# Kernel optimization log

Measured on AMD Instinct MI355X. Metric: run time of the kernel, lower is better.

## Reference

```python
import jax, jax.numpy as jnp
import numpy as np

N_POINTS = 32
N_HEADS = 4
EMBED = 256
TAU = 2.0


def _grid_sample_bilinear(val, gx, gy):
    # val: [N, C, H, W]; gx, gy: [N, Q, P] normalized coords in [-1, 1]
    # bilinear, padding_mode='zeros', align_corners=False
    N, C, H, W = val.shape
    ix = (gx + 1.0) * (W * 0.5) - 0.5
    iy = (gy + 1.0) * (H * 0.5) - 0.5
    x0 = jnp.floor(ix)
    y0 = jnp.floor(iy)
    x1 = x0 + 1.0
    y1 = y0 + 1.0
    wx1 = ix - x0
    wx0 = 1.0 - wx1
    wy1 = iy - y0
    wy0 = 1.0 - wy1
    gather = jax.vmap(lambda v, yy, xx: v[:, yy, xx])  # per-image advanced-index gather
    out = jnp.zeros((N, C) + gx.shape[1:], dtype=val.dtype)
    for xs, ys, wx, wy in ((x0, y0, wx0, wy0), (x1, y0, wx1, wy0),
                           (x0, y1, wx0, wy1), (x1, y1, wx1, wy1)):
        m = ((xs >= 0) & (xs < W) & (ys >= 0) & (ys < H)).astype(val.dtype) * wx * wy
        xi = jnp.clip(xs, 0, W - 1).astype(jnp.int32)
        yi = jnp.clip(ys, 0, H - 1).astype(jnp.int32)
        out = out + gather(val, yi, xi) * m[:, None]
    return out  # [N, C, Q, P]


def setup_inputs() -> dict:
    key = jax.random.key(0)
    ks = jax.random.split(key, 18)
    B, L = 2, 1000
    lvl_hw = [(256, 256), (128, 128), (64, 64), (32, 32)]
    inp = {}
    for i, (h, w) in enumerate(lvl_hw):
        inp[f'value{i}'] = jax.random.normal(ks[i], (B, EMBED, h, w), jnp.float32)
    inp['query_content'] = jax.random.normal(ks[4], (B, L, EMBED), jnp.float32)
    img = 1024.0
    xy = jax.random.uniform(ks[5], (B, L, 2), minval=0.0, maxval=img)
    z = jax.random.uniform(ks[6], (B, L, 1), minval=4.0, maxval=6.5)
    r = jax.random.uniform(ks[7], (B, L, 1), minval=-0.8, maxval=0.8)
    th = jax.random.uniform(ks[8], (B, L, 1), minval=-np.pi, maxval=np.pi)
    inp['query_xyzrt'] = jnp.concatenate([xy, z, r, th], axis=-1).astype(jnp.float32)
    inp['strides'] = jnp.array([4, 8, 16, 32], jnp.int32)
    s = 0.02
    inp['W_off'] = jax.random.normal(ks[9], (EMBED, N_HEADS * N_POINTS * 3)) * s
    inp['b_off'] = jax.random.normal(ks[10], (N_HEADS * N_POINTS * 3,)) * 0.2
    inp['W_ca1'] = jax.random.normal(ks[11], (EMBED, EMBED // 4)) * s
    inp['W_ca2'] = jax.random.normal(ks[12], (EMBED // 4, EMBED)) * s
    inp['W_sa1'] = jax.random.normal(ks[13], (EMBED, EMBED // 4)) * s
    inp['W_sa2'] = jax.random.normal(ks[14], (EMBED // 4, N_HEADS * N_POINTS)) * s
    inp['W_out'] = jax.random.normal(ks[15], (EMBED * N_POINTS, EMBED)) * s
    inp['b_out'] = jnp.zeros((EMBED,), jnp.float32)
    return inp


def reference(value0, value1, value2, value3, query_content, query_xyzrt, strides,
              W_off, b_off, W_ca1, W_ca2, W_sa1, W_sa2, W_out, b_out):
    values = [value0, value1, value2, value3]
    B, L, _ = query_content.shape
    P = N_HEADS * N_POINTS
    G = N_HEADS
    ch = EMBED // G

    # ---- make_sample_points ----
    offset = (query_content @ W_off + b_off).reshape(B, L, P, 3)
    roi_cc = query_xyzrt[..., :2]                      # [B,L,2]
    scale = 2.0 ** query_xyzrt[..., 2:3]
    ratio = 2.0 ** jnp.concatenate([query_xyzrt[..., 3:4] * -0.5,
                                    query_xyzrt[..., 3:4] * 0.5], axis=-1)
    roi_wh = scale * ratio                             # [B,L,2]
    theta = query_xyzrt[..., 4]
    c, s = jnp.cos(theta), jnp.sin(theta)
    R = jnp.stack([jnp.stack([c, -s], -1), jnp.stack([s, c], -1)], -2)  # [B,L,2,2]
    off_xy = offset[..., :2] * roi_wh[:, :, None, :]
    rot_xy = jnp.einsum('blpj,blij->blpi', off_xy, R)  # offset @ R^T
    sample_xy = roi_cc[:, :, None, :] + rot_xy         # [B,L,P,2] absolute coords
    sample_z = query_xyzrt[..., 2][:, :, None] + offset[..., 2]  # [B,L,P]

    # ---- level weights: sigmoid(-(z - log2(stride))^2 / tau) ----
    grid = jnp.log2(strides.astype(sample_z.dtype))    # [n_levels]
    lvl_w = jax.nn.sigmoid(-((sample_z[..., None] - grid) ** 2) / TAU)  # [B,L,P,n_lvl]

    # ---- multi-level rotated deformable sampling ----
    sampling_value = jnp.zeros((B, L, G, N_POINTS, ch), query_content.dtype)
    for lvl, v in enumerate(values):
        H, W = v.shape[2], v.shape[3]
        stride_f = strides[lvl].astype(sample_xy.dtype)
        mapping = jnp.stack([W * stride_f, H * stride_f])  # (x_extent, y_extent)
        norm_xy = sample_xy / mapping * 2.0 - 1.0          # [B,L,P,2] in [-1,1]
        # split points into head groups: [B,L,G,pts,2] -> [B*G, L, pts, 2]
        g_xy = norm_xy.reshape(B, L, G, N_POINTS, 2).transpose(0, 2, 1, 3, 4).reshape(B * G, L, N_POINTS, 2)
        v_g = v.reshape(B * G, ch, H, W)
        out = _grid_sample_bilinear(v_g, g_xy[..., 0], g_xy[..., 1])  # [B*G, ch, L, pts]
        w = lvl_w[..., lvl].reshape(B, L, G, N_POINTS).transpose(0, 2, 1, 3).reshape(B * G, 1, L, N_POINTS)
        out = out * w
        sampling_value = sampling_value + out.reshape(B, G, ch, L, N_POINTS).transpose(0, 3, 1, 4, 2)

    # ---- channel / spatial attention gates ----
    ca = jax.nn.sigmoid(jax.nn.relu(query_content @ W_ca1) @ W_ca2)
    ca = ca.reshape(B, L, G, 1, ch)
    sa = jax.nn.sigmoid(jax.nn.relu(query_content @ W_sa1) @ W_sa2)
    sa = sa.reshape(B, L, G, N_POINTS, 1)
    out = sampling_value * ca * sa
    out = out.reshape(B, L, G * N_POINTS * ch) @ W_out + b_out
    return out + query_content
```

## Files before the change

### kernel.cpp

```cpp
#include <hip/hip_runtime.h>

#define NQ    2000
#define KDIM  8192
#define EMB   256
#define MPAD  2048
#define SPLITK 8

typedef __attribute__((ext_vector_type(8))) short bf16x8;
typedef __attribute__((ext_vector_type(4))) float f32x4;

__device__ __forceinline__ float sigf(float x) { return 1.0f / (1.0f + __expf(-x)); }

__device__ __forceinline__ unsigned short f2bf(float x) {
    union { float f; unsigned int u; } v; v.f = x;
    unsigned int r = v.u + 0x7fffu + ((v.u >> 16) & 1u);
    return (unsigned short)(r >> 16);
}
__device__ __forceinline__ float bf2f(unsigned short h) {
    union { unsigned int u; float f; } v; v.u = ((unsigned int)h) << 16; return v.f;
}

__global__ __launch_bounds__(256) void trans_kernel(
    const float* __restrict__ v0, const float* __restrict__ v1,
    const float* __restrict__ v2, const float* __restrict__ v3,
    unsigned short* __restrict__ vt0, unsigned short* __restrict__ vt1,
    unsigned short* __restrict__ vt2, unsigned short* __restrict__ vt3,
    const float* __restrict__ Wout, unsigned short* __restrict__ Wtb,
    const float* __restrict__ Woff, const float* __restrict__ Wca1,
    const float* __restrict__ Wsa1,
    unsigned short* __restrict__ WH, unsigned short* __restrict__ WL,
    const float* __restrict__ qc,
    unsigned short* __restrict__ qcH, unsigned short* __restrict__ qcL)
{
    __shared__ float tile[64][33];
    int bid = blockIdx.x;
    const int t = threadIdx.x;

    if (bid < 21760) {
        const float* v; unsigned short* vt; int H;
        if (bid < 16384)      { v = v0; vt = vt0; H = 256; }
        else if (bid < 20480) { bid -= 16384; v = v1; vt = vt1; H = 128; }
        else if (bid < 21504) { bid -= 20480; v = v2; vt = vt2; H = 64; }
        else                  { bid -= 21504; v = v3; vt = vt3; H = 32; }
        const int y  = bid % H;            bid /= H;
        const int xt = bid % (H >> 5);     bid /= (H >> 5);
        const int ct = bid & 3;
        const int b  = bid >> 2;
        const float* src = v + ((size_t)(b * 256 + ct * 64) * H + y) * H + xt * 32;
        const int xi = t & 31;
        #pragma unroll
        for (int i = 0; i < 8; i++) {
            const int c = (t >> 5) + i * 8;
            tile[c][xi] = src[(size_t)c * H * H + xi];
        }
        __syncthreads();
        unsigned short* dst = vt + (((size_t)(b * H + y) * H + xt * 32) * 256) + ct * 64;
        const int ci = (t & 31) * 2;
        #pragma unroll
        for (int i = 0; i < 4; i++) {
            const int x2 = (t >> 5) + i * 8;
            ushort2 pk;
            pk.x = f2bf(tile[ci][x2]);
            pk.y = f2bf(tile[ci + 1][x2]);
            *(ushort2*)(dst + (size_t)x2 * 256 + ci) = pk;
        }
    } else if (bid < 23808) {
        const int local = bid - 21760;
        const int k0 = (local & 255) * 32, n0 = (local >> 8) * 32;
        float (*tl)[33] = tile;
        #pragma unroll
        for (int i = 0; i < 4; i++) {
            const int ki = (t >> 5) + i * 8;
            tl[ki][t & 31] = Wout[(size_t)(k0 + ki) * 256 + n0 + (t & 31)];
        }
        __syncthreads();
        #pragma unroll
        for (int i = 0; i < 4; i++) {
            const int ni = (t >> 5) + i * 8;
            const int ki = t & 31;
            Wtb[(size_t)(n0 + ni) * KDIM + k0 + ki] = f2bf(tl[ki][ni]);
        }
    } else if (bid < 24320) {
        const int n = bid - 23808;
        float val;
        if (n < 384)      val = Woff[(size_t)t * 384 + n];
        else if (n < 448) val = Wca1[(size_t)t * 64 + (n - 384)];
        else              val = Wsa1[(size_t)t * 64 + (n - 448)];
        const unsigned short hh = f2bf(val);
        WH[(size_t)n * 256 + t] = hh;
        WL[(size_t)n * 256 + t] = f2bf(val - bf2f(hh));
    } else {
        const int q = bid - 24320;
        const float val = (q < NQ) ? qc[(size_t)q * 256 + t] : 0.f;
        const unsigned short hh = f2bf(val);
        qcH[(size_t)q * 256 + t] = hh;
        qcL[(size_t)q * 256 + t] = f2bf(val - bf2f(hh));
    }
}

__global__ __launch_bounds__(256) void gemmA_kernel(
    const unsigned short* __restrict__ qcH, const unsigned short* __restrict__ qcL,
    const unsigned short* __restrict__ WH,  const unsigned short* __restrict__ WL,
    float* __restrict__ Hout)
{
    const int m0 = blockIdx.x * 64;
    const int n0 = blockIdx.y * 64;
    const int t  = threadIdx.x;
    const int w    = t >> 6;
    const int lane = t & 63;
    const int mw = (w & 1) * 32;
    const int nw = (w >> 1) * 32;
    const int quad = lane >> 4;
    const int l16  = lane & 15;

    f32x4 acc[2][2] = {};
    #pragma unroll
    for (int pass = 0; pass < 3; pass++) {
        const unsigned short* Ap = (pass == 2) ? qcL : qcH;
        const unsigned short* Bp = (pass == 1) ? WL : WH;
        const unsigned short* ar0 = Ap + (size_t)(m0 + mw + l16) * 256 + quad * 8;
        const unsigned short* ar1 = ar0 + 16 * 256;
        const unsigned short* br0 = Bp + (size_t)(n0 + nw + l16) * 256 + quad * 8;
        const unsigned short* br1 = br0 + 16 * 256;
        #pragma unroll
        for (int k = 0; k < 256; k += 32) {
            const bf16x8 a0 = *(const bf16x8*)(ar0 + k);
            const bf16x8 a1 = *(const bf16x8*)(ar1 + k);
            const bf16x8 b0 = *(const bf16x8*)(br0 + k);
            const bf16x8 b1 = *(const bf16x8*)(br1 + k);
            acc[0][0] = __builtin_amdgcn_mfma_f32_16x16x32_bf16(a0, b0, acc[0][0], 0, 0, 0);
            acc[0][1] = __builtin_amdgcn_mfma_f32_16x16x32_bf16(a0, b1, acc[0][1], 0, 0, 0);
            acc[1][0] = __builtin_amdgcn_mfma_f32_16x16x32_bf16(a1, b0, acc[1][0], 0, 0, 0);
            acc[1][1] = __builtin_amdgcn_mfma_f32_16x16x32_bf16(a1, b1, acc[1][1], 0, 0, 0);
        }
    }
    #pragma unroll
    for (int i = 0; i < 2; i++)
        #pragma unroll
        for (int j = 0; j < 2; j++) {
            const int n = n0 + nw + 16 * j + l16;
            #pragma unroll
            for (int r = 0; r < 4; r++) {
                const int m = m0 + mw + 16 * i + quad * 4 + r;
                Hout[(size_t)m * 512 + n] = acc[i][j][r];
            }
        }
}

__global__ __launch_bounds__(256) void finish_kernel(
    const float* __restrict__ Hbuf, const float* __restrict__ xyzrt,
    const float* __restrict__ boff,
    const float* __restrict__ Wca2, const float* __restrict__ Wsa2,
    float* __restrict__ qdata)
{
    const int q0 = blockIdx.x * 8;
    const int t  = threadIdx.x;
    __shared__ float hca[8][64];
    __shared__ float hsa[8][64];
    __shared__ float sas[8][128];

    for (int i = t; i < 1024; i += 256) {
        const int q = i >> 7, j = i & 127;
        const float v = fmaxf(Hbuf[(size_t)(q0 + q) * 512 + 384 + j], 0.f);
        if (j < 64) hca[q][j] = v; else hsa[q][j - 64] = v;
    }
    __syncthreads();

    {
        float acc[8] = {};
        for (int j = 0; j < 64; j++) {
            const float wv = Wca2[(size_t)j * 256 + t];
            #pragma unroll
            for (int q = 0; q < 8; q++) acc[q] = fmaf(hca[q][j], wv, acc[q]);
        }
        #pragma unroll
        for (int q = 0; q < 8; q++)
            qdata[(size_t)(q0 + q) * 1024 + 768 + t] = sigf(acc[q]);
    }
    {
        const int c  = t & 127;
        const int qb = (t >> 7) * 4;
        float acc[4] = {};
        for (int j = 0; j < 64; j++) {
            const float wv = Wsa2[(size_t)j * 128 + c];
            #pragma unroll
            for (int qq = 0; qq < 4; qq++) acc[qq] = fmaf(hsa[qb + qq][j], wv, acc[qq]);
        }
        #pragma unroll
        for (int qq = 0; qq < 4; qq++) sas[qb + qq][c] = sigf(acc[qq]);
    }
    __syncthreads();

    {
        const int p  = t & 127;
        const int qb = (t >> 7) * 4;
        #pragma unroll
        for (int qq = 0; qq < 4; qq++) {
            const int q = qb + qq;
            const float* hrow = Hbuf + (size_t)(q0 + q) * 512 + p * 3;
            const float o0 = hrow[0] + boff[p * 3 + 0];
            const float o1 = hrow[1] + boff[p * 3 + 1];
            const float o2 = hrow[2] + boff[p * 3 + 2];
            const float* xr = xyzrt + (size_t)(q0 + q) * 5;
            const float x = xr[0], y = xr[1], z = xr[2], r = xr[3], th = xr[4];
            const float sc  = exp2f(z);
            const float rw  = sc * exp2f(-0.5f * r);
            const float rh  = sc * exp2f( 0.5f * r);
            const float cth = __cosf(th), sth = __sinf(th);
            const float ox = o0 * rw;
            const float oy = o1 * rh;
            float* qd = qdata + (size_t)(q0 + q) * 1024;
            qd[p]       = x + cth * ox - sth * oy;
            qd[128 + p] = y + sth * ox + cth * oy;
            const float sz = z + o2;
            const float sa = sas[q][p];
            #pragma unroll
            for (int l = 0; l < 4; l++) {
                const float d = sz - (float)(2 + l);
                qd[256 + p * 4 + l] = sigf(-0.5f * d * d) * sa;
            }
        }
    }
}

__global__ __launch_bounds__(256) void sample_kernel(
    const unsigned short* __restrict__ v0, const unsigned short* __restrict__ v1,
    const unsigned short* __restrict__ v2, const unsigned short* __restrict__ v3,
    const float* __restrict__ qdata,
    unsigned short* __restrict__ X)
{
    const int wid  = blockIdx.x * 4 + (threadIdx.x >> 6);
    const int lane = threadIdx.x & 63;
    const int q  = wid >> 4;
    const int pb = (wid & 15) * 8;
    const int pt = lane >> 3;
    const int gp = pb + pt;
    const int g  = gp >> 5;
    const int c8 = (lane & 7) * 8;
    const int b  = (q >= 1000) ? 1 : 0;

    const float* qd = qdata + (size_t)q * 1024;
    const float px = qd[gp];
    const float py = qd[128 + gp];
    const float4 wl4 = *(const float4*)(qd + 256 + gp * 4);
    const float wlv[4] = { wl4.x, wl4.y, wl4.z, wl4.w };

    const unsigned short* vals[4] = { v0, v1, v2, v3 };
    const int cbase = g * 64 + c8;

    uint4 dv[16];
    float mv[16];
    #pragma unroll
    for (int l = 0; l < 4; l++) {
        const int   H   = 256 >> l;
        const float inv = 1.0f / (float)(4 << l);
        const float wl  = wlv[l];
        const float ix = px * inv - 0.5f;
        const float iy = py * inv - 0.5f;
        const float x0f = floorf(ix), y0f = floorf(iy);
        const int   x0 = (int)x0f,    y0 = (int)y0f;
        const float fx1 = ix - x0f, fx0 = 1.f - fx1;
        const float fy1 = iy - y0f, fy0 = 1.f - fy1;
        const bool xi0 = (x0 >= 0) & (x0 < H);
        const bool xi1 = (x0 + 1 >= 0) & (x0 + 1 < H);
        const bool yi0 = (y0 >= 0) & (y0 < H);
        const bool yi1 = (y0 + 1 >= 0) & (y0 + 1 < H);
        const int xc0 = min(max(x0, 0), H - 1);
        const int xc1 = min(max(x0 + 1, 0), H - 1);
        const int yc0 = min(max(y0, 0), H - 1);
        const int yc1 = min(max(y0 + 1, 0), H - 1);
        mv[l * 4 + 0] = (xi0 & yi0) ? wl * fx0 * fy0 : 0.f;
        mv[l * 4 + 1] = (xi1 & yi0) ? wl * fx1 * fy0 : 0.f;
        mv[l * 4 + 2] = (xi0 & yi1) ? wl * fx0 * fy1 : 0.f;
        mv[l * 4 + 3] = (xi1 & yi1) ? wl * fx1 * fy1 : 0.f;

        const unsigned short* base = vals[l] + (size_t)b * H * H * 256 + cbase;
        const int ry0 = yc0 * H, ry1 = yc1 * H;
        dv[l * 4 + 0] = *(const uint4*)(base + (size_t)(ry0 + xc0) * 256);
        dv[l * 4 + 1] = *(const uint4*)(base + (size_t)(ry0 + xc1) * 256);
        dv[l * 4 + 2] = *(const uint4*)(base + (size_t)(ry1 + xc0) * 256);
        dv[l * 4 + 3] = *(const uint4*)(base + (size_t)(ry1 + xc1) * 256);
    }

    float acc[8] = {};
    #pragma unroll
    for (int s = 0; s < 16; s++) {
        const unsigned int du[4] = { dv[s].x, dv[s].y, dv[s].z, dv[s].w };
        const float m = mv[s];
        #pragma unroll
        for (int i = 0; i < 4; i++) {
            union { unsigned int u; float f; } lo, hi;
            lo.u = du[i] << 16;
            hi.u = du[i] & 0xffff0000u;
            acc[2 * i]     = fmaf(m, lo.f, acc[2 * i]);
            acc[2 * i + 1] = fmaf(m, hi.f, acc[2 * i + 1]);
        }
    }

    const float* caf = qd + 768 + cbase;
    const float4 ca0 = *(const float4*)caf;
    const float4 ca1 = *(const float4*)(caf + 4);
    const float cav[8] = { ca0.x, ca0.y, ca0.z, ca0.w, ca1.x, ca1.y, ca1.z, ca1.w };
    uint4 o;
    unsigned int* op = (unsigned int*)&o;
    #pragma unroll
    for (int i = 0; i < 4; i++) {
        const unsigned int lo = f2bf(acc[2 * i] * cav[2 * i]);
        const unsigned int hi = f2bf(acc[2 * i + 1] * cav[2 * i + 1]);
        op[i] = lo | (hi << 16);
    }
    *(uint4*)(X + (size_t)q * KDIM + pb * 64 + lane * 8) = o;
}

__global__ __launch_bounds__(256) void gemm_kernel(
    const unsigned short* __restrict__ X,
    const unsigned short* __restrict__ Wt,
    float* __restrict__ part)
{
    const int m0 = blockIdx.x * 64;
    const int n0 = blockIdx.y * 64;
    const int z  = blockIdx.z;
    const int t  = threadIdx.x;
    const int w    = t >> 6;
    const int lane = t & 63;
    const int mw = (w & 1) * 32;
    const int nw = (w >> 1) * 32;
    const int quad = lane >> 4;
    const int l16  = lane & 15;

    const unsigned short* ar0 = X  + (size_t)(m0 + mw + l16) * KDIM + quad * 8;
    const unsigned short* ar1 = ar0 + (size_t)16 * KDIM;
    const unsigned short* br0 = Wt + (size_t)(n0 + nw + l16) * KDIM + quad * 8;
    const unsigned short* br1 = br0 + (size_t)16 * KDIM;

    f32x4 acc[2][2] = {};
    const int kbase = z * (KDIM / SPLITK);
    #pragma unroll 4
    for (int k = kbase; k < kbase + KDIM / SPLITK; k += 32) {
        const bf16x8 a0 = *(const bf16x8*)(ar0 + k);
        const bf16x8 a1 = *(const bf16x8*)(ar1 + k);
        const bf16x8 b0 = *(const bf16x8*)(br0 + k);
        const bf16x8 b1 = *(const bf16x8*)(br1 + k);
        acc[0][0] = __builtin_amdgcn_mfma_f32_16x16x32_bf16(a0, b0, acc[0][0], 0, 0, 0);
        acc[0][1] = __builtin_amdgcn_mfma_f32_16x16x32_bf16(a0, b1, acc[0][1], 0, 0, 0);
        acc[1][0] = __builtin_amdgcn_mfma_f32_16x16x32_bf16(a1, b0, acc[1][0], 0, 0, 0);
        acc[1][1] = __builtin_amdgcn_mfma_f32_16x16x32_bf16(a1, b1, acc[1][1], 0, 0, 0);
    }

    float* pz = part + (size_t)z * MPAD * EMB;
    #pragma unroll
    for (int i = 0; i < 2; i++)
        #pragma unroll
        for (int j = 0; j < 2; j++) {
            const int n = n0 + nw + 16 * j + l16;
            #pragma unroll
            for (int r = 0; r < 4; r++) {
                const int m = m0 + mw + 16 * i + quad * 4 + r;
                pz[(size_t)m * EMB + n] = acc[i][j][r];
            }
        }
}

__global__ __launch_bounds__(256) void reduce_kernel(
    const float* __restrict__ part, const float* __restrict__ qc,
    const float* __restrict__ bias, float* __restrict__ out)
{
    const int idx = blockIdx.x * 256 + threadIdx.x;
    if (idx >= NQ * 64) return;
    const int m  = idx >> 6;
    const int c4 = idx & 63;
    float4 a = ((const float4*)bias)[c4];
    const float4 qv = ((const float4*)qc)[(size_t)m * 64 + c4];
    a.x += qv.x; a.y += qv.y; a.z += qv.z; a.w += qv.w;
    #pragma unroll
    for (int z = 0; z < SPLITK; z++) {
        const float4 p = ((const float4*)part)[((size_t)z * MPAD + m) * 64 + c4];
        a.x += p.x; a.y += p.y; a.z += p.z; a.w += p.w;
    }
    ((float4*)out)[(size_t)m * 64 + c4] = a;
}

extern "C" void kernel_launch(void* const* d_in, const int* in_sizes, int n_in,
                              void* d_out, int out_size, void* d_ws, size_t ws_size,
                              hipStream_t stream) {
    (void)in_sizes; (void)n_in; (void)out_size; (void)ws_size;
    const float* v0    = (const float*)d_in[0];
    const float* v1    = (const float*)d_in[1];
    const float* v2    = (const float*)d_in[2];
    const float* v3    = (const float*)d_in[3];
    const float* qc    = (const float*)d_in[4];
    const float* xyzrt = (const float*)d_in[5];
    const float* Woff  = (const float*)d_in[7];
    const float* boff  = (const float*)d_in[8];
    const float* Wca1  = (const float*)d_in[9];
    const float* Wca2  = (const float*)d_in[10];
    const float* Wsa1  = (const float*)d_in[11];
    const float* Wsa2  = (const float*)d_in[12];
    const float* Wout  = (const float*)d_in[13];
    const float* bout  = (const float*)d_in[14];
    float* out = (float*)d_out;

    char* p = (char*)d_ws;
    float* qdata = (float*)p;                 p += (size_t)NQ * 1024 * 4;
    unsigned short* Xb = (unsigned short*)p;  p += (size_t)MPAD * KDIM * 2;
    unsigned short* vt0 = (unsigned short*)p; p += (size_t)2 * 256 * 256 * 256 * 2;
    unsigned short* vt1 = (unsigned short*)p; p += (size_t)2 * 128 * 128 * 256 * 2;
    unsigned short* vt2 = (unsigned short*)p; p += (size_t)2 * 64 * 64 * 256 * 2;
    unsigned short* vt3 = (unsigned short*)p; p += (size_t)2 * 32 * 32 * 256 * 2;
    unsigned short* Wtb = (unsigned short*)p; p += (size_t)EMB * KDIM * 2;
    float* partb = (float*)p;                 p += (size_t)SPLITK * MPAD * EMB * 4;
    float* Hbuf = (float*)p;                  p += (size_t)MPAD * 512 * 4;
    unsigned short* qcH = (unsigned short*)p; p += (size_t)MPAD * 256 * 2;
    unsigned short* qcL = (unsigned short*)p; p += (size_t)MPAD * 256 * 2;
    unsigned short* WHb = (unsigned short*)p; p += (size_t)512 * 256 * 2;
    unsigned short* WLb = (unsigned short*)p;

    trans_kernel<<<26368, 256, 0, stream>>>(v0, v1, v2, v3, vt0, vt1, vt2, vt3,
                                            Wout, Wtb, Woff, Wca1, Wsa1,
                                            WHb, WLb, qc, qcH, qcL);
    gemmA_kernel<<<dim3(MPAD / 64, 8), 256, 0, stream>>>(qcH, qcL, WHb, WLb, Hbuf);
    finish_kernel<<<NQ / 8, 256, 0, stream>>>(Hbuf, xyzrt, boff, Wca2, Wsa2, qdata);
    sample_kernel<<<(NQ * 128) / (4 * 8), 256, 0, stream>>>(vt0, vt1, vt2, vt3, qdata, Xb);
    gemm_kernel<<<dim3(MPAD / 64, EMB / 64, SPLITK), 256, 0, stream>>>(Xb, Wtb, partb);
    reduce_kernel<<<(NQ * 64 + 255) / 256, 256, 0, stream>>>(partb, qc, bout, out);
}
```

Baseline: 390.1 us.

## Fuse bilinear sampling with output GEMM via LDS-staged per-head tiles

Merges the sampling kernel and the split-K output GEMM into one kernel. Each block samples 16 queries for one head group, writes the bf16 tile into swizzled LDS, then multiplies it against that head's slice of W_out with MFMA. Per-head partials are written out and summed by the reduce kernel, which now reads 4 partials instead of 8. This removes the global round trip of the large intermediate X matrix and one kernel launch. In exchange, the W_out slices are re-read from global by every block, each block uses 64KB of LDS, and the sampling and GEMM phases no longer overlap across blocks.

Result: faster. 380.3 us (-2.5%).

```diff
diff --git a/kernel.cpp b/kernel.cpp
--- a/kernel.cpp
+++ b/kernel.cpp
@@ -4,7 +4,7 @@
 #define KDIM  8192
 #define EMB   256
 #define MPAD  2048
-#define SPLITK 8
+#define NH    4
 
 typedef __attribute__((ext_vector_type(8))) short bf16x8;
 typedef __attribute__((ext_vector_type(4))) float f32x4;
@@ -223,142 +223,136 @@
     }
 }
 
-__global__ __launch_bounds__(256) void sample_kernel(
+__global__ __launch_bounds__(512, 4) void fused_kernel(
     const unsigned short* __restrict__ v0, const unsigned short* __restrict__ v1,
     const unsigned short* __restrict__ v2, const unsigned short* __restrict__ v3,
     const float* __restrict__ qdata,
-    unsigned short* __restrict__ X)
-{
-    const int wid  = blockIdx.x * 4 + (threadIdx.x >> 6);
-    const int lane = threadIdx.x & 63;
-    const int q  = wid >> 4;
-    const int pb = (wid & 15) * 8;
-    const int pt = lane >> 3;
-    const int gp = pb + pt;
-    const int g  = gp >> 5;
-    const int c8 = (lane & 7) * 8;
-    const int b  = (q >= 1000) ? 1 : 0;
-
-    const float* qd = qdata + (size_t)q * 1024;
-    const float px = qd[gp];
-    const float py = qd[128 + gp];
-    const float4 wl4 = *(const float4*)(qd + 256 + gp * 4);
-    const float wlv[4] = { wl4.x, wl4.y, wl4.z, wl4.w };
-
-    const unsigned short* vals[4] = { v0, v1, v2, v3 };
-    const int cbase = g * 64 + c8;
-
-    uint4 dv[16];
-    float mv[16];
-    #pragma unroll
-    for (int l = 0; l < 4; l++) {
-        const int   H   = 256 >> l;
-        const float inv = 1.0f / (float)(4 << l);
-        const float wl  = wlv[l];
-        const float ix = px * inv - 0.5f;
-        const float iy = py * inv - 0.5f;
-        const float x0f = floorf(ix), y0f = floorf(iy);
-        const int   x0 = (int)x0f,    y0 = (int)y0f;
-        const float fx1 = ix - x0f, fx0 = 1.f - fx1;
-        const float fy1 = iy - y0f, fy0 = 1.f - fy1;
-        const bool xi0 = (x0 >= 0) & (x0 < H);
-        const bool xi1 = (x0 + 1 >= 0) & (x0 + 1 < H);
-        const bool yi0 = (y0 >= 0) & (y0 < H);
-        const bool yi1 = (y0 + 1 >= 0) & (y0 + 1 < H);
-        const int xc0 = min(max(x0, 0), H - 1);
-        const int xc1 = min(max(x0 + 1, 0), H - 1);
-        const int yc0 = min(max(y0, 0), H - 1);
-        const int yc1 = min(max(y0 + 1, 0), H - 1);
-        mv[l * 4 + 0] = (xi0 & yi0) ? wl * fx0 * fy0 : 0.f;
-        mv[l * 4 + 1] = (xi1 & yi0) ? wl * fx1 * fy0 : 0.f;
-        mv[l * 4 + 2] = (xi0 & yi1) ? wl * fx0 * fy1 : 0.f;
-        mv[l * 4 + 3] = (xi1 & yi1) ? wl * fx1 * fy1 : 0.f;
-
-        const unsigned short* base = vals[l] + (size_t)b * H * H * 256 + cbase;
-        const int ry0 = yc0 * H, ry1 = yc1 * H;
-        dv[l * 4 + 0] = *(const uint4*)(base + (size_t)(ry0 + xc0) * 256);
-        dv[l * 4 + 1] = *(const uint4*)(base + (size_t)(ry0 + xc1) * 256);
-        dv[l * 4 + 2] = *(const uint4*)(base + (size_t)(ry1 + xc0) * 256);
-        dv[l * 4 + 3] = *(const uint4*)(base + (size_t)(ry1 + xc1) * 256);
-    }
-
-    float acc[8] = {};
-    #pragma unroll
-    for (int s = 0; s < 16; s++) {
-        const unsigned int du[4] = { dv[s].x, dv[s].y, dv[s].z, dv[s].w };
-        const float m = mv[s];
-        #pragma unroll
-        for (int i = 0; i < 4; i++) {
-            union { unsigned int u; float f; } lo, hi;
-            lo.u = du[i] << 16;
-            hi.u = du[i] & 0xffff0000u;
-            acc[2 * i]     = fmaf(m, lo.f, acc[2 * i]);
-            acc[2 * i + 1] = fmaf(m, hi.f, acc[2 * i + 1]);
-        }
-    }
-
-    const float* caf = qd + 768 + cbase;
-    const float4 ca0 = *(const float4*)caf;
-    const float4 ca1 = *(const float4*)(caf + 4);
-    const float cav[8] = { ca0.x, ca0.y, ca0.z, ca0.w, ca1.x, ca1.y, ca1.z, ca1.w };
-    uint4 o;
-    unsigned int* op = (unsigned int*)&o;
-    #pragma unroll
-    for (int i = 0; i < 4; i++) {
-        const unsigned int lo = f2bf(acc[2 * i] * cav[2 * i]);
-        const unsigned int hi = f2bf(acc[2 * i + 1] * cav[2 * i + 1]);
-        op[i] = lo | (hi << 16);
-    }
-    *(uint4*)(X + (size_t)q * KDIM + pb * 64 + lane * 8) = o;
-}
-
-__global__ __launch_bounds__(256) void gemm_kernel(
-    const unsigned short* __restrict__ X,
     const unsigned short* __restrict__ Wt,
     float* __restrict__ part)
 {
-    const int m0 = blockIdx.x * 64;
-    const int n0 = blockIdx.y * 64;
-    const int z  = blockIdx.z;
+    __shared__ __align__(16) unsigned char Alds[16 * 4096];
+    const int q0 = blockIdx.x * 16;
+    const int g  = blockIdx.y;
     const int t  = threadIdx.x;
     const int w    = t >> 6;
     const int lane = t & 63;
-    const int mw = (w & 1) * 32;
-    const int nw = (w >> 1) * 32;
-    const int quad = lane >> 4;
-    const int l16  = lane & 15;
-
-    const unsigned short* ar0 = X  + (size_t)(m0 + mw + l16) * KDIM + quad * 8;
-    const unsigned short* ar1 = ar0 + (size_t)16 * KDIM;
-    const unsigned short* br0 = Wt + (size_t)(n0 + nw + l16) * KDIM + quad * 8;
-    const unsigned short* br1 = br0 + (size_t)16 * KDIM;
-
-    f32x4 acc[2][2] = {};
-    const int kbase = z * (KDIM / SPLITK);
-    #pragma unroll 4
-    for (int k = kbase; k < kbase + KDIM / SPLITK; k += 32) {
-        const bf16x8 a0 = *(const bf16x8*)(ar0 + k);
-        const bf16x8 a1 = *(const bf16x8*)(ar1 + k);
-        const bf16x8 b0 = *(const bf16x8*)(br0 + k);
-        const bf16x8 b1 = *(const bf16x8*)(br1 + k);
-        acc[0][0] = __builtin_amdgcn_mfma_f32_16x16x32_bf16(a0, b0, acc[0][0], 0, 0, 0);
-        acc[0][1] = __builtin_amdgcn_mfma_f32_16x16x32_bf16(a0, b1, acc[0][1], 0, 0, 0);
-        acc[1][0] = __builtin_amdgcn_mfma_f32_16x16x32_bf16(a1, b0, acc[1][0], 0, 0, 0);
-        acc[1][1] = __builtin_amdgcn_mfma_f32_16x16x32_bf16(a1, b1, acc[1][1], 0, 0, 0);
-    }
-
-    float* pz = part + (size_t)z * MPAD * EMB;
-    #pragma unroll
-    for (int i = 0; i < 2; i++)
-        #pragma unroll
-        for (int j = 0; j < 2; j++) {
-            const int n = n0 + nw + 16 * j + l16;
-            #pragma unroll
-            for (int r = 0; r < 4; r++) {
-                const int m = m0 + mw + 16 * i + quad * 4 + r;
-                pz[(size_t)m * EMB + n] = acc[i][j][r];
+
+    const unsigned short* vals[4] = { v0, v1, v2, v3 };
+
+    {
+        const int pt = lane >> 3;
+        const int ck = lane & 7;
+        const int p  = (w & 3) * 8 + pt;
+        const int cbase = g * 64 + ck * 8;
+        const int gp = g * 32 + p;
+
+        #pragma unroll
+        for (int r = 0; r < 8; r++) {
+            const int qloc = r * 2 + (w >> 2);
+            const int q = q0 + qloc;
+            const int b = (q >= 1000) ? 1 : 0;
+            const float* qd = qdata + (size_t)q * 1024;
+            const float px = qd[gp];
+            const float py = qd[128 + gp];
+            const float4 wl4 = *(const float4*)(qd + 256 + gp * 4);
+            const float wlv[4] = { wl4.x, wl4.y, wl4.z, wl4.w };
+
+            float acc[8] = {};
+            #pragma unroll
+            for (int half = 0; half < 2; half++) {
+                uint4 dv[8];
+                float mv[8];
+                #pragma unroll
+                for (int li = 0; li < 2; li++) {
+                    const int l = half * 2 + li;
+                    const int   H   = 256 >> l;
+                    const float inv = 1.0f / (float)(4 << l);
+                    const float wl  = wlv[l];
+                    const float ix = px * inv - 0.5f;
+                    const float iy = py * inv - 0.5f;
+                    const float x0f = floorf(ix), y0f = floorf(iy);
+                    const int   x0 = (int)x0f,    y0 = (int)y0f;
+                    const float fx1 = ix - x0f, fx0 = 1.f - fx1;
+                    const float fy1 = iy - y0f, fy0 = 1.f - fy1;
+                    const bool xi0 = (x0 >= 0) & (x0 < H);
+                    const bool xi1 = (x0 + 1 >= 0) & (x0 + 1 < H);
+                    const bool yi0 = (y0 >= 0) & (y0 < H);
+                    const bool yi1 = (y0 + 1 >= 0) & (y0 + 1 < H);
+                    const int xc0 = min(max(x0, 0), H - 1);
+                    const int xc1 = min(max(x0 + 1, 0), H - 1);
+                    const int yc0 = min(max(y0, 0), H - 1);
+                    const int yc1 = min(max(y0 + 1, 0), H - 1);
+                    mv[li * 4 + 0] = (xi0 & yi0) ? wl * fx0 * fy0 : 0.f;
+                    mv[li * 4 + 1] = (xi1 & yi0) ? wl * fx1 * fy0 : 0.f;
+                    mv[li * 4 + 2] = (xi0 & yi1) ? wl * fx0 * fy1 : 0.f;
+                    mv[li * 4 + 3] = (xi1 & yi1) ? wl * fx1 * fy1 : 0.f;
+                    const unsigned short* base = vals[l] + (size_t)b * H * H * 256 + cbase;
+                    const int ry0 = yc0 * H, ry1 = yc1 * H;
+                    dv[li * 4 + 0] = *(const uint4*)(base + (size_t)(ry0 + xc0) * 256);
+                    dv[li * 4 + 1] = *(const uint4*)(base + (size_t)(ry0 + xc1) * 256);
+                    dv[li * 4 + 2] = *(const uint4*)(base + (size_t)(ry1 + xc0) * 256);
+                    dv[li * 4 + 3] = *(const uint4*)(base + (size_t)(ry1 + xc1) * 256);
+                }
+                #pragma unroll
+                for (int s = 0; s < 8; s++) {
+                    const unsigned int du[4] = { dv[s].x, dv[s].y, dv[s].z, dv[s].w };
+                    const float m = mv[s];
+                    #pragma unroll
+                    for (int i = 0; i < 4; i++) {
+                        union { unsigned int u; float f; } lo, hi;
+                        lo.u = du[i] << 16;
+                        hi.u = du[i] & 0xffff0000u;
+                        acc[2 * i]     = fmaf(m, lo.f, acc[2 * i]);
+                        acc[2 * i + 1] = fmaf(m, hi.f, acc[2 * i + 1]);
+                    }
+                }
             }
-        }
+
+            const float* caf = qd + 768 + cbase;
+            const float4 ca0 = *(const float4*)caf;
+            const float4 ca1 = *(const float4*)(caf + 4);
+            const float cav[8] = { ca0.x, ca0.y, ca0.z, ca0.w, ca1.x, ca1.y, ca1.z, ca1.w };
+            uint4 o;
+            unsigned int* op = (unsigned int*)&o;
+            #pragma unroll
+            for (int i = 0; i < 4; i++) {
+                const unsigned int lo = f2bf(acc[2 * i] * cav[2 * i]);
+                const unsigned int hi = f2bf(acc[2 * i + 1] * cav[2 * i + 1]);
+                op[i] = lo | (hi << 16);
+            }
+            const unsigned int C = (unsigned)(p * 8 + ck);
+            const unsigned int byteoff = (unsigned)qloc * 4096u + ((C ^ (unsigned)(qloc & 7)) * 16u);
+            *(uint4*)(Alds + byteoff) = o;
+        }
+    }
+    __syncthreads();
+
+    {
+        const int quad = lane >> 4;
+        const int l16  = lane & 15;
+        const unsigned short* br0 = Wt + (size_t)(w * 32 + l16) * KDIM + g * 2048 + quad * 8;
+        const unsigned short* br1 = br0 + (size_t)16 * KDIM;
+        const unsigned char* a_base = Alds + l16 * 4096;
+        const unsigned int axor = (unsigned)(l16 & 7);
+
+        f32x4 acc0 = {}, acc1 = {};
+        #pragma unroll 8
+        for (int kit = 0; kit < 64; kit++) {
+            const bf16x8 a  = *(const bf16x8*)(a_base + (((unsigned)(kit * 4 + quad) ^ axor) * 16u));
+            const bf16x8 b0 = *(const bf16x8*)(br0 + kit * 32);
+            const bf16x8 b1 = *(const bf16x8*)(br1 + kit * 32);
+            acc0 = __builtin_amdgcn_mfma_f32_16x16x32_bf16(a, b0, acc0, 0, 0, 0);
+            acc1 = __builtin_amdgcn_mfma_f32_16x16x32_bf16(a, b1, acc1, 0, 0, 0);
+        }
+
+        float* pz = part + ((size_t)g * MPAD + q0) * EMB;
+        #pragma unroll
+        for (int r = 0; r < 4; r++) {
+            const int m = quad * 4 + r;
+            pz[(size_t)m * EMB + w * 32 + l16]      = acc0[r];
+            pz[(size_t)m * EMB + w * 32 + 16 + l16] = acc1[r];
+        }
+    }
 }
 
 __global__ __launch_bounds__(256) void reduce_kernel(
@@ -373,7 +367,7 @@
     const float4 qv = ((const float4*)qc)[(size_t)m * 64 + c4];
     a.x += qv.x; a.y += qv.y; a.z += qv.z; a.w += qv.w;
     #pragma unroll
-    for (int z = 0; z < SPLITK; z++) {
+    for (int z = 0; z < NH; z++) {
         const float4 p = ((const float4*)part)[((size_t)z * MPAD + m) * 64 + c4];
         a.x += p.x; a.y += p.y; a.z += p.z; a.w += p.w;
     }
@@ -408,19 +402,19 @@
     unsigned short* vt2 = (unsigned short*)p; p += (size_t)2 * 64 * 64 * 256 * 2;
     unsigned short* vt3 = (unsigned short*)p; p += (size_t)2 * 32 * 32 * 256 * 2;
     unsigned short* Wtb = (unsigned short*)p; p += (size_t)EMB * KDIM * 2;
-    float* partb = (float*)p;                 p += (size_t)SPLITK * MPAD * EMB * 4;
+    float* partb = (float*)p;                 p += (size_t)8 * MPAD * EMB * 4;
     float* Hbuf = (float*)p;                  p += (size_t)MPAD * 512 * 4;
     unsigned short* qcH = (unsigned short*)p; p += (size_t)MPAD * 256 * 2;
     unsigned short* qcL = (unsigned short*)p; p += (size_t)MPAD * 256 * 2;
     unsigned short* WHb = (unsigned short*)p; p += (size_t)512 * 256 * 2;
     unsigned short* WLb = (unsigned short*)p;
+    (void)Xb;
 
     trans_kernel<<<26368, 256, 0, stream>>>(v0, v1, v2, v3, vt0, vt1, vt2, vt3,
                                             Wout, Wtb, Woff, Wca1, Wsa1,
                                             WHb, WLb, qc, qcH, qcL);
     gemmA_kernel<<<dim3(MPAD / 64, 8), 256, 0, stream>>>(qcH, qcL, WHb, WLb, Hbuf);
     finish_kernel<<<NQ / 8, 256, 0, stream>>>(Hbuf, xyzrt, boff, Wca2, Wsa2, qdata);
-    sample_kernel<<<(NQ * 128) / (4 * 8), 256, 0, stream>>>(vt0, vt1, vt2, vt3, qdata, Xb);
-    gemm_kernel<<<dim3(MPAD / 64, EMB / 64, SPLITK), 256, 0, stream>>>(Xb, Wtb, partb);
+    fused_kernel<<<dim3(NQ / 16, NH), 512, 0, stream>>>(vt0, vt1, vt2, vt3, qdata, Wtb, partb);
     reduce_kernel<<<(NQ * 64 + 255) / 256, 256, 0, stream>>>(partb, qc, bout, out);
 }
```
